# Performance work log

Hardware: AMD Instinct MI355X
Metric: run time of the kernel (lower is better)

Reference implementation:

```python
import jax, jax.numpy as jnp
import numpy as np

D_MODEL, FF_DIM = 1024, 2048
N_SHARED, N_ROUTED, TOP_K = 1, 8, 2
BATCH, SEQ = 2, 2048


def setup_inputs() -> dict:
    key = jax.random.key(0)
    ks = jax.random.split(key, 8)
    init = lambda k, shape: (jax.random.normal(k, shape, jnp.float32) * 0.02)
    x = jax.random.normal(ks[0], (BATCH, SEQ, D_MODEL), jnp.float32)
    Wg = init(ks[1], (D_MODEL, N_ROUTED))                 # gate
    Ws1 = init(ks[2], (D_MODEL, FF_DIM))                  # shared expert (N_SHARED=1)
    Ws3 = init(ks[3], (D_MODEL, FF_DIM))
    Ws2 = init(ks[4], (FF_DIM, D_MODEL))
    We1 = init(ks[5], (N_ROUTED, D_MODEL, FF_DIM))        # routed experts, stacked
    We3 = init(ks[6], (N_ROUTED, D_MODEL, FF_DIM))
    We2 = init(ks[7], (N_ROUTED, FF_DIM, D_MODEL))
    return {"x": x, "Wg": Wg, "Ws1": Ws1, "Ws3": Ws3, "Ws2": Ws2,
            "We1": We1, "We3": We3, "We2": We2}


def reference(x, Wg, Ws1, Ws3, Ws2, We1, We3, We2):
    B, S, d = x.shape
    E = Wg.shape[1]
    xf = x.reshape(-1, d)                                  # [T, d]
    T = xf.shape[0]

    # sigmoid gate + top-k, normalized over selected experts
    gates = jax.nn.sigmoid(xf @ Wg)                        # [T, E]
    vals, idx = jax.lax.top_k(gates, TOP_K)                # [T, K]
    vals = vals / vals.sum(axis=-1, keepdims=True)
    # dense per-expert weights (scatter normalized top-k probs)
    w = jnp.zeros((T, E), x.dtype).at[jnp.arange(T)[:, None], idx].add(vals)  # [T, E]

    # shared expert SwiGLU
    shared = (jax.nn.silu(xf @ Ws1) * (xf @ Ws3)) @ Ws2    # [T, d]

    # routed experts: same math as the torch loop (compute all, mask by w)
    h = jax.nn.silu(jnp.einsum('td,edf->tef', xf, We1)) \
        * jnp.einsum('td,edf->tef', xf, We3)               # [T, E, ff]
    routed = jnp.einsum('tef,efd,te->td', h, We2, w)       # [T, d]

    out = (shared + routed) / (N_SHARED + TOP_K)
    return out.reshape(B, S, d)
```

## Files before the change

### kernel.cpp

```cpp
#include <hip/hip_runtime.h>
#include <stdint.h>

#define TTOK 4096
#define DM   1024
#define FF   2048
#define NE   8

typedef __attribute__((ext_vector_type(8))) short short8;
typedef __attribute__((ext_vector_type(8))) unsigned short ushort8;
typedef __attribute__((ext_vector_type(4))) float f32x4;

#define OFF_XB      0ull
#define OFF_WB13    (OFF_XB      + (size_t)TTOK*DM*2)
#define OFF_WB2     (OFF_WB13    + (size_t)9*4096*1024*2)
#define OFF_H       (OFF_WB2     + (size_t)9*1024*2048*2)
#define OFF_CONTRIB (OFF_H       + (size_t)12288*2048*2)
#define OFF_TOPKW   (OFF_CONTRIB + (size_t)8192*1024*4)
#define OFF_TOPKI   (OFF_TOPKW   + (size_t)TTOK*2*4)
#define OFF_SLOTTOK (OFF_TOPKI   + (size_t)TTOK*2*4)
#define OFF_TOKSLOT (OFF_SLOTTOK + (size_t)TTOK*2*4)
#define OFF_COUNTS  (OFF_TOKSLOT + (size_t)TTOK*2*4)
#define WS_NEEDED   (OFF_COUNTS + 256)

#define VMWAIT(N) asm volatile("s_waitcnt vmcnt(" #N ")" ::: "memory")
#define LGKM0()   asm volatile("s_waitcnt lgkmcnt(0)" ::: "memory")
#define BAR()     __builtin_amdgcn_s_barrier()
#define SCHED0()  __builtin_amdgcn_sched_barrier(0)

__device__ __forceinline__ unsigned short f2bf(float f) {
  unsigned u = __float_as_uint(f);
  return (unsigned short)((u + 0x7FFFu + ((u >> 16) & 1u)) >> 16);
}

__device__ __forceinline__ void async16(const void* g, void* l) {
  __builtin_amdgcn_global_load_lds(
      (const __attribute__((address_space(1))) void*)g,
      (__attribute__((address_space(3))) void*)l, 16, 0, 0);
}

__global__ void k_gatecvt(const float* __restrict__ x, const float* __restrict__ Wg,
                          float* __restrict__ topkw, int* __restrict__ topki,
                          unsigned short* __restrict__ xb) {
  int wave = threadIdx.x >> 6;
  int lane = threadIdx.x & 63;
  int t = blockIdx.x * 4 + wave;
  float acc[NE];
#pragma unroll
  for (int e = 0; e < NE; e++) acc[e] = 0.f;
  const float* xr = x + (size_t)t * DM;
  unsigned short* xbr = xb + (size_t)t * DM;
#pragma unroll
  for (int i = 0; i < 4; i++) {
    int k = i * 256 + lane * 4;
    f32x4 xv = *(const f32x4*)(xr + k);
    unsigned short o0 = f2bf(xv[0]), o1 = f2bf(xv[1]), o2 = f2bf(xv[2]), o3 = f2bf(xv[3]);
    unsigned long long pk = (unsigned long long)o0 | ((unsigned long long)o1 << 16) |
                            ((unsigned long long)o2 << 32) | ((unsigned long long)o3 << 48);
    *(unsigned long long*)(xbr + k) = pk;
#pragma unroll
    for (int j = 0; j < 4; j++) {
      const float* wr = Wg + (size_t)(k + j) * NE;
#pragma unroll
      for (int e = 0; e < NE; e++) acc[e] += xv[j] * wr[e];
    }
  }
#pragma unroll
  for (int e = 0; e < NE; e++) {
#pragma unroll
    for (int off = 32; off >= 1; off >>= 1) acc[e] += __shfl_xor(acc[e], off, 64);
  }
  if (lane == 0) {
    float g[NE];
#pragma unroll
    for (int e = 0; e < NE; e++) g[e] = 1.f / (1.f + __expf(-acc[e]));
    int i1 = -1, i2 = -1;
    float m1 = -1e30f, m2 = -1e30f;
#pragma unroll
    for (int e = 0; e < NE; e++) {
      float v = g[e];
      if (v > m1) { m2 = m1; i2 = i1; m1 = v; i1 = e; }
      else if (v > m2) { m2 = v; i2 = e; }
    }
    float s = m1 + m2;
    topkw[t * 2 + 0] = m1 / s;
    topkw[t * 2 + 1] = m2 / s;
    topki[t * 2 + 0] = i1;
    topki[t * 2 + 1] = i2;
  }
}

__global__ void k_route(const int* __restrict__ topki, int* __restrict__ counts_g,
                        int* __restrict__ offs_g, int* __restrict__ slot_token,
                        int* __restrict__ token_slot) {
  __shared__ int cnt[NE], off[NE], fill[NE];
  int tid = threadIdx.x;
  if (tid < NE) { cnt[tid] = 0; fill[tid] = 0; }
  __syncthreads();
  for (int t = tid; t < TTOK; t += 1024) {
    atomicAdd(&cnt[topki[t * 2 + 0]], 1);
    atomicAdd(&cnt[topki[t * 2 + 1]], 1);
  }
  __syncthreads();
  if (tid == 0) {
    int s = 0;
    for (int e = 0; e < NE; e++) { off[e] = s; s += cnt[e]; }
  }
  __syncthreads();
  if (tid < NE) { counts_g[tid] = cnt[tid]; offs_g[tid] = off[tid]; }
  for (int t = tid; t < TTOK; t += 1024) {
#pragma unroll
    for (int k = 0; k < 2; k++) {
      int e = topki[t * 2 + k];
      int pos = atomicAdd(&fill[e], 1);
      int slot = off[e] + pos;
      slot_token[slot] = t;
      token_slot[t * 2 + k] = slot;
    }
  }
}

__global__ void k_t13(const float* __restrict__ We1, const float* __restrict__ We3,
                      const float* __restrict__ Ws1, const float* __restrict__ Ws3,
                      unsigned short* __restrict__ wb13) {
  __shared__ float tile[64][68];
  int z = blockIdx.z;
  unsigned short* dst = wb13 + (size_t)z * 4096 * 1024;
  int r0 = blockIdx.y * 64;
  int c0 = blockIdx.x * 64;
  int tid = threadIdx.x;
  int r = tid >> 2, q = tid & 3;
  int nn = tid >> 2, g = tid & 3;

  const float* srcs[2] = {(blockIdx.z < 8) ? We1 + (size_t)z * DM * FF : Ws1,
                          (blockIdx.z < 8) ? We3 + (size_t)z * DM * FF : Ws3};
#pragma unroll
  for (int m = 0; m < 2; m++) {
    const float* src = srcs[m] + (size_t)(r0 + r) * FF + c0;
#pragma unroll
    for (int i = 0; i < 4; i++)
      *(f32x4*)&tile[r][i * 16 + q * 4] = *(const f32x4*)(src + i * 16 + q * 4);
    __syncthreads();
    int n = c0 + nn;
    int d = ((n >> 4) << 5) + (n & 15) + m * 16;
    ushort8 o0, o1;
#pragma unroll
    for (int j = 0; j < 8; j++) o0[j] = f2bf(tile[g * 16 + j][nn]);
#pragma unroll
    for (int j = 0; j < 8; j++) o1[j] = f2bf(tile[g * 16 + 8 + j][nn]);
    unsigned short* dp = dst + (size_t)d * 1024 + r0 + g * 16;
    *(ushort8*)dp = o0;
    *(ushort8*)(dp + 8) = o1;
    __syncthreads();
  }
}

__global__ void k_t2(const float* __restrict__ We2, const float* __restrict__ Ws2,
                     unsigned short* __restrict__ wb2) {
  __shared__ float tile[64][68];
  int z = blockIdx.z;
  const float* src0 = (z < 8) ? We2 + (size_t)z * FF * DM : Ws2;
  unsigned short* dst = wb2 + (size_t)z * 1024 * 2048;
  int r0 = blockIdx.y * 64;
  int c0 = blockIdx.x * 64;
  int tid = threadIdx.x;
  int r = tid >> 2, q = tid & 3;
  int nn = tid >> 2, g = tid & 3;

  const float* src = src0 + (size_t)(r0 + r) * DM + c0;
#pragma unroll
  for (int i = 0; i < 4; i++)
    *(f32x4*)&tile[r][i * 16 + q * 4] = *(const f32x4*)(src + i * 16 + q * 4);
  __syncthreads();
  ushort8 o0, o1;
#pragma unroll
  for (int j = 0; j < 8; j++) o0[j] = f2bf(tile[g * 16 + j][nn]);
#pragma unroll
  for (int j = 0; j < 8; j++) o1[j] = f2bf(tile[g * 16 + 8 + j][nn]);
  unsigned short* dp = dst + (size_t)(c0 + nn) * 2048 + r0 + g * 16;
  *(ushort8*)dp = o0;
  *(ushort8*)(dp + 8) = o1;
}

template <bool G13, int K, int NBROW>
__global__ __launch_bounds__(512, 2) void k_gemm(
    const unsigned short* __restrict__ A, const unsigned short* __restrict__ B,
    unsigned short* __restrict__ Hout, float* __restrict__ Cout, float* __restrict__ Dout,
    const int* __restrict__ slot_token, const int* __restrict__ offs,
    const int* __restrict__ counts) {
  __shared__ unsigned short lds[2][2][2][8192];
  const int NT = K / 64;

  int e = blockIdx.z;
  int seg, cnt;
  if (e == 8) { seg = 8192; cnt = 4096; }
  else        { seg = offs[e]; cnt = counts[e]; }
  int m0 = blockIdx.y * 256;
  if (m0 >= cnt) return;
  int bn = blockIdx.x;

  int tid = threadIdx.x, lane = tid & 63, w = tid >> 6;

  int srcslot = (((tid & 7) ^ ((tid >> 3) & 7)) << 4);
  const char* aptr[2][2];
  const char* bptr[2][2];
#pragma unroll
  for (int half = 0; half < 2; half++)
#pragma unroll
    for (int j = 0; j < 2; j++) {
      int rl = half * 128 + j * 64 + (tid >> 3);
      int r = m0 + rl; if (r > cnt - 1) r = cnt - 1;
      long tok;
      if (G13) tok = (e == 8) ? (long)r : (long)slot_token[seg + r];
      else     tok = (long)(seg + r);
      aptr[half][j] = (const char*)A + ((size_t)tok * K) * 2 + srcslot;
      int br = bn * 256 + rl;
      bptr[half][j] = (const char*)B + (((size_t)e * NBROW + br) * K) * 2 + srcslot;
    }

#define STG(b, op, half, kt) do {                                           \
    const char* _p0 = (op ? bptr : aptr)[half][0] + (size_t)(kt) * 128;     \
    const char* _p1 = (op ? bptr : aptr)[half][1] + (size_t)(kt) * 128;     \
    async16(_p0, &lds[b][op][half][(size_t)w * 512]);                       \
    async16(_p1, &lds[b][op][half][4096 + (size_t)w * 512]);                \
  } while (0)

  int wr = w >> 2, wc = w & 3, wch = wc >> 1;
  int s0 = (((0 + (lane >> 4)) ^ (lane & 7)) << 4);
  int s1 = (((4 + (lane >> 4)) ^ (lane & 7)) << 4);

  f32x4 acc[8][4];
#pragma unroll
  for (int i = 0; i < 8; i++)
#pragma unroll
    for (int j = 0; j < 4; j++) acc[i][j] = (f32x4){0.f, 0.f, 0.f, 0.f};

  short8 Af[2][2], Bf[4][2];

#define DO_PHASE(LA, LB, qq, STG_STMT, WAIT_STMT) do {                        \
    if (qq == 0) {                                                            \
      _Pragma("unroll") for (int nf = 0; nf < 4; nf++) {                      \
        int rb = ((wc & 1) * 64 + nf * 16 + (lane & 15)) * 128;               \
        Bf[nf][0] = *(const short8*)((LB) + rb + s0);                         \
        Bf[nf][1] = *(const short8*)((LB) + rb + s1);                         \
      }                                                                       \
    }                                                                         \
    _Pragma("unroll") for (int m2 = 0; m2 < 2; m2++) {                        \
      int ra = (((qq) * 2 + m2) * 16 + (lane & 15)) * 128;                    \
      Af[m2][0] = *(const short8*)((LA) + ra + s0);                           \
      Af[m2][1] = *(const short8*)((LA) + ra + s1);                           \
    }                                                                         \
    STG_STMT;                                                                 \
    BAR();                                                                    \
    LGKM0();                                                                  \
    SCHED0();                                                                 \
    __builtin_amdgcn_s_setprio(1);                                            \
    _Pragma("unroll") for (int m2 = 0; m2 < 2; m2++)                          \
      _Pragma("unroll") for (int nf = 0; nf < 4; nf++) {                      \
        acc[(qq) * 2 + m2][nf] = __builtin_amdgcn_mfma_f32_16x16x32_bf16(     \
            Af[m2][0], Bf[nf][0], acc[(qq) * 2 + m2][nf], 0, 0, 0);           \
        acc[(qq) * 2 + m2][nf] = __builtin_amdgcn_mfma_f32_16x16x32_bf16(     \
            Af[m2][1], Bf[nf][1], acc[(qq) * 2 + m2][nf], 0, 0, 0);           \
      }                                                                       \
    __builtin_amdgcn_s_setprio(0);                                            \
    WAIT_STMT;                                                                \
    BAR();                                                                    \
  } while (0)

  STG(0, 1, 0, 0);
  STG(0, 1, 1, 0);
  STG(0, 0, 0, 0);
  STG(0, 0, 1, 0);
  STG(1, 1, 0, 1);
  VMWAIT(2);
  BAR();

  const char* LA0 = (const char*)&lds[0][0][wr][0];
  const char* LB0 = (const char*)&lds[0][1][wch][0];
  const char* LA1 = (const char*)&lds[1][0][wr][0];
  const char* LB1 = (const char*)&lds[1][1][wch][0];

  for (int it = 0; it < NT / 2; ++it) {
    int t1 = 2 * it + 1;
    int n2 = (2 * it + 2 < NT) ? 2 * it + 2 : NT - 1;
    int n3 = (2 * it + 3 < NT) ? 2 * it + 3 : NT - 1;
    DO_PHASE(LA0, LB0, 0, STG(1, 1, 1, t1), );
    DO_PHASE(LA0, LB0, 1, STG(1, 0, 0, t1), );
    DO_PHASE(LA0, LB0, 2, STG(1, 0, 1, t1), );
    DO_PHASE(LA0, LB0, 3, STG(0, 1, 0, n2), VMWAIT(2));
    DO_PHASE(LA1, LB1, 0, STG(0, 1, 1, n2), );
    DO_PHASE(LA1, LB1, 1, STG(0, 0, 0, n2), );
    DO_PHASE(LA1, LB1, 2, STG(0, 0, 1, n2), );
    DO_PHASE(LA1, LB1, 3, STG(1, 1, 0, n3), VMWAIT(2));
  }
  VMWAIT(0);
#undef DO_PHASE
#undef STG

  if (G13) {
#pragma unroll
    for (int mi = 0; mi < 8; mi++)
#pragma unroll
      for (int j = 0; j < 2; j++)
#pragma unroll
        for (int q = 0; q < 4; q++) {
          int rl = wr * 128 + mi * 16 + (lane >> 4) * 4 + q;
          if (m0 + rl < cnt) {
            float s1v = acc[mi][2 * j][q], s3v = acc[mi][2 * j + 1][q];
            float h = (s1v / (1.f + __expf(-s1v))) * s3v;
            int ffcol = (bn * 8 + wc * 2 + j) * 16 + (lane & 15);
            Hout[(size_t)(seg + m0 + rl) * 2048 + ffcol] = f2bf(h);
          }
        }
  } else {
#pragma unroll
    for (int mi = 0; mi < 8; mi++)
#pragma unroll
      for (int nf = 0; nf < 4; nf++)
#pragma unroll
        for (int q = 0; q < 4; q++) {
          int rl = wr * 128 + mi * 16 + (lane >> 4) * 4 + q;
          if (m0 + rl < cnt) {
            int col = bn * 256 + wc * 64 + nf * 16 + (lane & 15);
            if (e == 8) Dout[(size_t)(m0 + rl) * 1024 + col] = acc[mi][nf][q];
            else        Cout[(size_t)(seg + m0 + rl) * 1024 + col] = acc[mi][nf][q];
          }
        }
  }
}

__global__ void k_combine(float* __restrict__ out, const float* __restrict__ contrib,
                          const int* __restrict__ token_slot, const float* __restrict__ topkw) {
  int t = blockIdx.x;
  int c = threadIdx.x * 4;
  int s0 = token_slot[t * 2 + 0], s1 = token_slot[t * 2 + 1];
  float w0 = topkw[t * 2 + 0], w1 = topkw[t * 2 + 1];
  float* po = out + (size_t)t * DM + c;
  const float* p0 = contrib + (size_t)s0 * DM + c;
  const float* p1 = contrib + (size_t)s1 * DM + c;
  f32x4 vo = *(f32x4*)po;
  f32x4 v0 = *(const f32x4*)p0;
  f32x4 v1 = *(const f32x4*)p1;
#pragma unroll
  for (int i = 0; i < 4; i++)
    vo[i] = (vo[i] + w0 * v0[i] + w1 * v1[i]) * (1.f / 3.f);
  *(f32x4*)po = vo;
}

extern "C" void kernel_launch(void* const* d_in, const int* in_sizes, int n_in,
                              void* d_out, int out_size, void* d_ws, size_t ws_size,
                              hipStream_t stream) {
  const float* x   = (const float*)d_in[0];
  const float* Wg  = (const float*)d_in[1];
  const float* Ws1 = (const float*)d_in[2];
  const float* Ws3 = (const float*)d_in[3];
  const float* Ws2 = (const float*)d_in[4];
  const float* We1 = (const float*)d_in[5];
  const float* We3 = (const float*)d_in[6];
  const float* We2 = (const float*)d_in[7];
  float* out = (float*)d_out;

  if (ws_size < WS_NEEDED) return;

  char* w = (char*)d_ws;
  unsigned short* xb   = (unsigned short*)(w + OFF_XB);
  unsigned short* wb13 = (unsigned short*)(w + OFF_WB13);
  unsigned short* wb2  = (unsigned short*)(w + OFF_WB2);
  unsigned short* H    = (unsigned short*)(w + OFF_H);
  float* contrib       = (float*)(w + OFF_CONTRIB);
  float* topkw         = (float*)(w + OFF_TOPKW);
  int* topki           = (int*)(w + OFF_TOPKI);
  int* slot_token      = (int*)(w + OFF_SLOTTOK);
  int* token_slot      = (int*)(w + OFF_TOKSLOT);
  int* counts          = (int*)(w + OFF_COUNTS);
  int* offs            = counts + 16;

  k_gatecvt<<<TTOK / 4, 256, 0, stream>>>(x, Wg, topkw, topki, xb);
  k_route<<<1, 1024, 0, stream>>>(topki, counts, offs, slot_token, token_slot);
  k_t13<<<dim3(FF / 64, DM / 64, 9), 256, 0, stream>>>(We1, We3, Ws1, Ws3, wb13);
  k_t2<<<dim3(DM / 64, FF / 64, 9), 256, 0, stream>>>(We2, Ws2, wb2);

  k_gemm<true, 1024, 4096><<<dim3(16, 16, 9), 512, 0, stream>>>(
      xb, wb13, H, nullptr, nullptr, slot_token, offs, counts);
  k_gemm<false, 2048, 1024><<<dim3(4, 16, 9), 512, 0, stream>>>(
      H, wb2, nullptr, contrib, out, slot_token, offs, counts);

  k_combine<<<TTOK, 256, 0, stream>>>(out, contrib, token_slot, topkw);
}
```

Before: 320.1 us.

## Pad expert segments to tile size and flatten grouped GEMM grid

Routing now pads each expert's token segment to a multiple of 256 and zero-fills the slot table, so GEMM blocks map from a flat 1D row-tile index to an expert without per-row bounds checks. The grid shrinks from 9 z-slices of 16 row tiles each (many empty blocks exit early) to 56 row tiles covering the padded routed segments plus shared rows. The LDS layout and staging pipeline are also restructured: A tiles are staged as a 256-row block, B fragments are preread once per k-tile, and the contrib buffer reuses the wb13 region to shrink the workspace. Padding rows do redundant compute, and the early-exit test now compares against the total padded length.

```diff
diff --git a/kernel.cpp b/kernel.cpp
--- a/kernel.cpp
+++ b/kernel.cpp
@@ -5,6 +5,8 @@
 #define DM   1024
 #define FF   2048
 #define NE   8
+#define SHSEG 10240
+#define HROWS 14336
 
 typedef __attribute__((ext_vector_type(8))) short short8;
 typedef __attribute__((ext_vector_type(8))) unsigned short ushort8;
@@ -14,13 +16,13 @@
 #define OFF_WB13    (OFF_XB      + (size_t)TTOK*DM*2)
 #define OFF_WB2     (OFF_WB13    + (size_t)9*4096*1024*2)
 #define OFF_H       (OFF_WB2     + (size_t)9*1024*2048*2)
-#define OFF_CONTRIB (OFF_H       + (size_t)12288*2048*2)
-#define OFF_TOPKW   (OFF_CONTRIB + (size_t)8192*1024*4)
+#define OFF_CONTRIB OFF_WB13
+#define OFF_TOPKW   (OFF_H       + (size_t)HROWS*2048*2)
 #define OFF_TOPKI   (OFF_TOPKW   + (size_t)TTOK*2*4)
 #define OFF_SLOTTOK (OFF_TOPKI   + (size_t)TTOK*2*4)
-#define OFF_TOKSLOT (OFF_SLOTTOK + (size_t)TTOK*2*4)
-#define OFF_COUNTS  (OFF_TOKSLOT + (size_t)TTOK*2*4)
-#define WS_NEEDED   (OFF_COUNTS + 256)
+#define OFF_TOKSLOT (OFF_SLOTTOK + (size_t)SHSEG*4)
+#define OFF_OFFS    (OFF_TOKSLOT + (size_t)TTOK*2*4)
+#define WS_NEEDED   (OFF_OFFS + 64)
 
 #define VMWAIT(N) asm volatile("s_waitcnt vmcnt(" #N ")" ::: "memory")
 #define LGKM0()   asm volatile("s_waitcnt lgkmcnt(0)" ::: "memory")
@@ -89,9 +91,8 @@
   }
 }
 
-__global__ void k_route(const int* __restrict__ topki, int* __restrict__ counts_g,
-                        int* __restrict__ offs_g, int* __restrict__ slot_token,
-                        int* __restrict__ token_slot) {
+__global__ void k_route(const int* __restrict__ topki, int* __restrict__ offs_g,
+                        int* __restrict__ slot_token, int* __restrict__ token_slot) {
   __shared__ int cnt[NE], off[NE], fill[NE];
   int tid = threadIdx.x;
   if (tid < NE) { cnt[tid] = 0; fill[tid] = 0; }
@@ -103,10 +104,13 @@
   __syncthreads();
   if (tid == 0) {
     int s = 0;
-    for (int e = 0; e < NE; e++) { off[e] = s; s += cnt[e]; }
-  }
-  __syncthreads();
-  if (tid < NE) { counts_g[tid] = cnt[tid]; offs_g[tid] = off[tid]; }
+    for (int e = 0; e < NE; e++) { off[e] = s; s += (cnt[e] + 255) & ~255; }
+    offs_g[8] = s;
+  }
+  __syncthreads();
+  if (tid < NE) offs_g[tid] = off[tid];
+  for (int s = tid; s < SHSEG; s += 1024) slot_token[s] = 0;
+  __syncthreads();
   for (int t = tid; t < TTOK; t += 1024) {
 #pragma unroll
     for (int k = 0; k < 2; k++) {
@@ -185,47 +189,57 @@
 __global__ __launch_bounds__(512, 2) void k_gemm(
     const unsigned short* __restrict__ A, const unsigned short* __restrict__ B,
     unsigned short* __restrict__ Hout, float* __restrict__ Cout, float* __restrict__ Dout,
-    const int* __restrict__ slot_token, const int* __restrict__ offs,
-    const int* __restrict__ counts) {
-  __shared__ unsigned short lds[2][2][2][8192];
+    const int* __restrict__ slot_token, const int* __restrict__ offs) {
+  __shared__ unsigned short As[2][256 * 64];
+  __shared__ unsigned short Bs[2][2][128 * 64];
   const int NT = K / 64;
 
-  int e = blockIdx.z;
-  int seg, cnt;
-  if (e == 8) { seg = 8192; cnt = 4096; }
-  else        { seg = offs[e]; cnt = counts[e]; }
-  int m0 = blockIdx.y * 256;
-  if (m0 >= cnt) return;
+  int my = blockIdx.y;
+  bool shd = (my >= 40);
+  int base = (shd ? my - 40 : my) * 256;
+  int e = 8;
+  if (!shd) {
+    if (base >= offs[8]) return;
+    e = 0;
+    while (e < 7 && base >= offs[e + 1]) ++e;
+  }
   int bn = blockIdx.x;
-
   int tid = threadIdx.x, lane = tid & 63, w = tid >> 6;
 
   int srcslot = (((tid & 7) ^ ((tid >> 3) & 7)) << 4);
-  const char* aptr[2][2];
-  const char* bptr[2][2];
-#pragma unroll
-  for (int half = 0; half < 2; half++)
-#pragma unroll
-    for (int j = 0; j < 2; j++) {
-      int rl = half * 128 + j * 64 + (tid >> 3);
-      int r = m0 + rl; if (r > cnt - 1) r = cnt - 1;
-      long tok;
-      if (G13) tok = (e == 8) ? (long)r : (long)slot_token[seg + r];
-      else     tok = (long)(seg + r);
-      aptr[half][j] = (const char*)A + ((size_t)tok * K) * 2 + srcslot;
-      int br = bn * 256 + rl;
-      bptr[half][j] = (const char*)B + (((size_t)e * NBROW + br) * K) * 2 + srcslot;
-    }
-
-#define STG(b, op, half, kt) do {                                           \
-    const char* _p0 = (op ? bptr : aptr)[half][0] + (size_t)(kt) * 128;     \
-    const char* _p1 = (op ? bptr : aptr)[half][1] + (size_t)(kt) * 128;     \
-    async16(_p0, &lds[b][op][half][(size_t)w * 512]);                       \
-    async16(_p1, &lds[b][op][half][4096 + (size_t)w * 512]);                \
+  unsigned aoff[4];
+#pragma unroll
+  for (int u = 0; u < 4; u++) {
+    int rl = u * 32 + (w & 3) * 8 + ((w >> 2) << 7) + (lane >> 3);
+    long row;
+    if (G13) row = shd ? (long)(base + rl) : (long)slot_token[base + rl];
+    else     row = (long)((shd ? SHSEG : 0) + base + rl);
+    aoff[u] = (unsigned)((size_t)row * K * 2) + srcslot;
+  }
+  unsigned boff[2];
+#pragma unroll
+  for (int half = 0; half < 2; half++) {
+    int br = bn * 256 + half * 128 + (tid >> 3);
+    boff[half] = (unsigned)(((size_t)e * NBROW + br) * K * 2) + srcslot;
+  }
+  const char* Abase = (const char*)A;
+  const char* Bbase = (const char*)B;
+
+#define A_STG(b, u, kt) \
+  async16(Abase + aoff[u] + (kt) * 128, \
+          &As[b][((u) * 32 + (w & 3) * 8 + ((w >> 2) << 7)) * 64])
+#define B_STG(b, half, kt) do { \
+    async16(Bbase + boff[half] + (size_t)(kt) * 128, &Bs[b][half][(w * 8) * 64]); \
+    async16(Bbase + boff[half] + (size_t)64 * K * 2 + (size_t)(kt) * 128, \
+            &Bs[b][half][(64 + w * 8) * 64]); \
   } while (0)
 
   int wr = w >> 2, wc = w & 3, wch = wc >> 1;
-  int s0 = (((0 + (lane >> 4)) ^ (lane & 7)) << 4);
+  const char* LA0 = (const char*)&As[0][0] + (wr * 128 + (lane & 15)) * 128;
+  const char* LA1 = (const char*)&As[1][0] + (wr * 128 + (lane & 15)) * 128;
+  const char* LB0 = (const char*)&Bs[0][wch][0] + ((wc & 1) * 64 + (lane & 15)) * 128;
+  const char* LB1 = (const char*)&Bs[1][wch][0] + ((wc & 1) * 64 + (lane & 15)) * 128;
+  int s0 = (((lane >> 4) ^ (lane & 7)) << 4);
   int s1 = (((4 + (lane >> 4)) ^ (lane & 7)) << 4);
 
   f32x4 acc[8][4];
@@ -234,69 +248,64 @@
 #pragma unroll
     for (int j = 0; j < 4; j++) acc[i][j] = (f32x4){0.f, 0.f, 0.f, 0.f};
 
-  short8 Af[2][2], Bf[4][2];
-
-#define DO_PHASE(LA, LB, qq, STG_STMT, WAIT_STMT) do {                        \
-    if (qq == 0) {                                                            \
-      _Pragma("unroll") for (int nf = 0; nf < 4; nf++) {                      \
-        int rb = ((wc & 1) * 64 + nf * 16 + (lane & 15)) * 128;               \
-        Bf[nf][0] = *(const short8*)((LB) + rb + s0);                         \
-        Bf[nf][1] = *(const short8*)((LB) + rb + s1);                         \
-      }                                                                       \
-    }                                                                         \
-    _Pragma("unroll") for (int m2 = 0; m2 < 2; m2++) {                        \
-      int ra = (((qq) * 2 + m2) * 16 + (lane & 15)) * 128;                    \
-      Af[m2][0] = *(const short8*)((LA) + ra + s0);                           \
-      Af[m2][1] = *(const short8*)((LA) + ra + s1);                           \
-    }                                                                         \
-    STG_STMT;                                                                 \
-    BAR();                                                                    \
-    LGKM0();                                                                  \
-    SCHED0();                                                                 \
-    __builtin_amdgcn_s_setprio(1);                                            \
-    _Pragma("unroll") for (int m2 = 0; m2 < 2; m2++)                          \
-      _Pragma("unroll") for (int nf = 0; nf < 4; nf++) {                      \
-        acc[(qq) * 2 + m2][nf] = __builtin_amdgcn_mfma_f32_16x16x32_bf16(     \
-            Af[m2][0], Bf[nf][0], acc[(qq) * 2 + m2][nf], 0, 0, 0);           \
-        acc[(qq) * 2 + m2][nf] = __builtin_amdgcn_mfma_f32_16x16x32_bf16(     \
-            Af[m2][1], Bf[nf][1], acc[(qq) * 2 + m2][nf], 0, 0, 0);           \
-      }                                                                       \
-    __builtin_amdgcn_s_setprio(0);                                            \
-    WAIT_STMT;                                                                \
-    BAR();                                                                    \
+  short8 Bf[4][2];
+
+#define PREREAD(LBx) do { \
+    _Pragma("unroll") for (int nf = 0; nf < 4; nf++) { \
+      Bf[nf][0] = *(const short8*)((LBx) + nf * 2048 + s0); \
+      Bf[nf][1] = *(const short8*)((LBx) + nf * 2048 + s1); \
+    } \
   } while (0)
 
-  STG(0, 1, 0, 0);
-  STG(0, 1, 1, 0);
-  STG(0, 0, 0, 0);
-  STG(0, 0, 1, 0);
-  STG(1, 1, 0, 1);
-  VMWAIT(2);
+#define PHASE(LAx, q, STGS, TAIL) do { \
+    short8 Af0k0 = *(const short8*)((LAx) + ((q) * 2 + 0) * 2048 + s0); \
+    short8 Af0k1 = *(const short8*)((LAx) + ((q) * 2 + 0) * 2048 + s1); \
+    short8 Af1k0 = *(const short8*)((LAx) + ((q) * 2 + 1) * 2048 + s0); \
+    short8 Af1k1 = *(const short8*)((LAx) + ((q) * 2 + 1) * 2048 + s1); \
+    STGS; \
+    BAR(); LGKM0(); SCHED0(); \
+    __builtin_amdgcn_s_setprio(1); \
+    _Pragma("unroll") for (int nf = 0; nf < 4; nf++) { \
+      acc[(q) * 2 + 0][nf] = __builtin_amdgcn_mfma_f32_16x16x32_bf16(Af0k0, Bf[nf][0], acc[(q) * 2 + 0][nf], 0, 0, 0); \
+      acc[(q) * 2 + 0][nf] = __builtin_amdgcn_mfma_f32_16x16x32_bf16(Af0k1, Bf[nf][1], acc[(q) * 2 + 0][nf], 0, 0, 0); \
+      acc[(q) * 2 + 1][nf] = __builtin_amdgcn_mfma_f32_16x16x32_bf16(Af1k0, Bf[nf][0], acc[(q) * 2 + 1][nf], 0, 0, 0); \
+      acc[(q) * 2 + 1][nf] = __builtin_amdgcn_mfma_f32_16x16x32_bf16(Af1k1, Bf[nf][1], acc[(q) * 2 + 1][nf], 0, 0, 0); \
+    } \
+    __builtin_amdgcn_s_setprio(0); \
+    TAIL; \
+    BAR(); \
+  } while (0)
+
+  B_STG(0, 0, 0); B_STG(0, 1, 0);
+  A_STG(0, 0, 0); A_STG(0, 1, 0); A_STG(0, 2, 0); A_STG(0, 3, 0);
+  B_STG(1, 0, 1); B_STG(1, 1, 1);
+  A_STG(1, 0, 1); A_STG(1, 1, 1);
+  VMWAIT(6);
   BAR();
-
-  const char* LA0 = (const char*)&lds[0][0][wr][0];
-  const char* LB0 = (const char*)&lds[0][1][wch][0];
-  const char* LA1 = (const char*)&lds[1][0][wr][0];
-  const char* LB1 = (const char*)&lds[1][1][wch][0];
-
-  for (int it = 0; it < NT / 2; ++it) {
-    int t1 = 2 * it + 1;
-    int n2 = (2 * it + 2 < NT) ? 2 * it + 2 : NT - 1;
-    int n3 = (2 * it + 3 < NT) ? 2 * it + 3 : NT - 1;
-    DO_PHASE(LA0, LB0, 0, STG(1, 1, 1, t1), );
-    DO_PHASE(LA0, LB0, 1, STG(1, 0, 0, t1), );
-    DO_PHASE(LA0, LB0, 2, STG(1, 0, 1, t1), );
-    DO_PHASE(LA0, LB0, 3, STG(0, 1, 0, n2), VMWAIT(2));
-    DO_PHASE(LA1, LB1, 0, STG(0, 1, 1, n2), );
-    DO_PHASE(LA1, LB1, 1, STG(0, 0, 0, n2), );
-    DO_PHASE(LA1, LB1, 2, STG(0, 0, 1, n2), );
-    DO_PHASE(LA1, LB1, 3, STG(1, 1, 0, n3), VMWAIT(2));
+  PREREAD(LB0);
+
+  const int NIT = NT / 2;
+  for (int it = 0; it < NIT; ++it) {
+    int kt1 = 2 * it + 1;
+    int kt2 = 2 * it + 2; if (kt2 > NT - 1) kt2 = NT - 1;
+    int kt3 = 2 * it + 3; if (kt3 > NT - 1) kt3 = NT - 1;
+    PHASE(LA0, 0, { A_STG(1, 2, kt1); A_STG(1, 3, kt1); }, {});
+    PHASE(LA0, 1, { B_STG(0, 0, kt2); }, {});
+    PHASE(LA0, 2, { B_STG(0, 1, kt2); }, {});
+    PHASE(LA0, 3, { A_STG(0, 0, kt2); A_STG(0, 1, kt2); }, { VMWAIT(6); PREREAD(LB1); });
+    PHASE(LA1, 0, { A_STG(0, 2, kt2); A_STG(0, 3, kt2); }, {});
+    PHASE(LA1, 1, { B_STG(1, 0, kt3); }, {});
+    PHASE(LA1, 2, { B_STG(1, 1, kt3); }, {});
+    PHASE(LA1, 3, { A_STG(1, 0, kt3); A_STG(1, 1, kt3); }, { VMWAIT(6); PREREAD(LB0); });
   }
   VMWAIT(0);
-#undef DO_PHASE
-#undef STG
+#undef PHASE
+#undef PREREAD
+#undef A_STG
+#undef B_STG
 
   if (G13) {
+    size_t hbase = (size_t)(shd ? SHSEG : 0) + base;
 #pragma unroll
     for (int mi = 0; mi < 8; mi++)
 #pragma unroll
@@ -304,12 +313,10 @@
 #pragma unroll
         for (int q = 0; q < 4; q++) {
           int rl = wr * 128 + mi * 16 + (lane >> 4) * 4 + q;
-          if (m0 + rl < cnt) {
-            float s1v = acc[mi][2 * j][q], s3v = acc[mi][2 * j + 1][q];
-            float h = (s1v / (1.f + __expf(-s1v))) * s3v;
-            int ffcol = (bn * 8 + wc * 2 + j) * 16 + (lane & 15);
-            Hout[(size_t)(seg + m0 + rl) * 2048 + ffcol] = f2bf(h);
-          }
+          float v1 = acc[mi][2 * j][q], v3 = acc[mi][2 * j + 1][q];
+          float h = (v1 / (1.f + __expf(-v1))) * v3;
+          int ffcol = (bn * 8 + wc * 2 + j) * 16 + (lane & 15);
+          Hout[(hbase + rl) * 2048 + ffcol] = f2bf(h);
         }
   } else {
 #pragma unroll
@@ -319,11 +326,9 @@
 #pragma unroll
         for (int q = 0; q < 4; q++) {
           int rl = wr * 128 + mi * 16 + (lane >> 4) * 4 + q;
-          if (m0 + rl < cnt) {
-            int col = bn * 256 + wc * 64 + nf * 16 + (lane & 15);
-            if (e == 8) Dout[(size_t)(m0 + rl) * 1024 + col] = acc[mi][nf][q];
-            else        Cout[(size_t)(seg + m0 + rl) * 1024 + col] = acc[mi][nf][q];
-          }
+          int col = bn * 256 + wc * 64 + nf * 16 + (lane & 15);
+          if (shd) Dout[(size_t)(base + rl) * 1024 + col] = acc[mi][nf][q];
+          else     Cout[(size_t)(base + rl) * 1024 + col] = acc[mi][nf][q];
         }
   }
 }
@@ -371,18 +376,17 @@
   int* topki           = (int*)(w + OFF_TOPKI);
   int* slot_token      = (int*)(w + OFF_SLOTTOK);
   int* token_slot      = (int*)(w + OFF_TOKSLOT);
-  int* counts          = (int*)(w + OFF_COUNTS);
-  int* offs            = counts + 16;
+  int* offs            = (int*)(w + OFF_OFFS);
 
   k_gatecvt<<<TTOK / 4, 256, 0, stream>>>(x, Wg, topkw, topki, xb);
-  k_route<<<1, 1024, 0, stream>>>(topki, counts, offs, slot_token, token_slot);
+  k_route<<<1, 1024, 0, stream>>>(topki, offs, slot_token, token_slot);
   k_t13<<<dim3(FF / 64, DM / 64, 9), 256, 0, stream>>>(We1, We3, Ws1, Ws3, wb13);
   k_t2<<<dim3(DM / 64, FF / 64, 9), 256, 0, stream>>>(We2, Ws2, wb2);
 
-  k_gemm<true, 1024, 4096><<<dim3(16, 16, 9), 512, 0, stream>>>(
-      xb, wb13, H, nullptr, nullptr, slot_token, offs, counts);
-  k_gemm<false, 2048, 1024><<<dim3(4, 16, 9), 512, 0, stream>>>(
-      H, wb2, nullptr, contrib, out, slot_token, offs, counts);
+  k_gemm<true, 1024, 4096><<<dim3(16, 56, 1), 512, 0, stream>>>(
+      xb, wb13, H, nullptr, nullptr, slot_token, offs);
+  k_gemm<false, 2048, 1024><<<dim3(4, 56, 1), 512, 0, stream>>>(
+      H, wb2, nullptr, contrib, out, slot_token, offs);
 
   k_combine<<<TTOK, 256, 0, stream>>>(out, contrib, token_slot, topkw);
 }
```

Measured after the change: 324.3 us. Within noise of the previous version (+1.3%).
